# Performance work log

Measured on AMD Instinct MI355X. Metric: run time of the kernel, lower is better.

## Reference

```python
import jax, jax.numpy as jnp
import numpy as np

N_HEAD = 16


def setup_inputs() -> dict:
    key = jax.random.key(0)
    ks = jax.random.split(key, 4)
    B, S, E = 1, 4096, 1024
    x = jax.random.normal(ks[0], (B, S, E), dtype=jnp.float32)
    # causal mask: True where attention is DISALLOWED (upper triangle)
    masked_matrix = ~jnp.tril(jnp.ones((S, S), dtype=bool))[None, None]
    Wqkv = jax.random.normal(ks[1], (E, 3 * E), dtype=jnp.float32) * (1.0 / np.sqrt(E))
    bqkv = jnp.zeros((3 * E,), dtype=jnp.float32)
    Wp = jax.random.normal(ks[2], (E, E), dtype=jnp.float32) * (1.0 / np.sqrt(E))
    bp = jnp.zeros((E,), dtype=jnp.float32)
    return {"x": x, "masked_matrix": masked_matrix, "Wqkv": Wqkv, "bqkv": bqkv,
            "Wp": Wp, "bp": bp}


def reference(x, masked_matrix, Wqkv, bqkv, Wp, bp):
    B, S, E = x.shape
    H = N_HEAD
    D = E // H
    qkv = x @ Wqkv + bqkv                        # [B,S,3E]
    q, k, v = jnp.split(qkv, 3, axis=-1)
    q = q.reshape(B, S, H, D).transpose(0, 2, 1, 3)  # [B,H,S,D]
    k = k.reshape(B, S, H, D).transpose(0, 2, 1, 3)
    v = v.reshape(B, S, H, D).transpose(0, 2, 1, 3)
    # NOTE: source applies NO 1/sqrt(D) scaling — kept faithful.
    att = jnp.einsum('bhqd,bhkd->bhqk', q, k)    # [B,H,S,S]
    att = jnp.where(masked_matrix, jnp.float32(-jnp.inf), att)
    att = jax.nn.softmax(att, axis=-1)
    res = jnp.einsum('bhqk,bhkd->bhqd', att, v)  # [B,H,S,D]
    res = res.transpose(0, 2, 1, 3).reshape(B, S, E)
    return res @ Wp + bp
```

## Files before the change

### kernel.cpp

```cpp
#include <hip/hip_runtime.h>
#include <hip/hip_bf16.h>
#include <math.h>

#define S_LEN 4096
#define EMB   1024
#define NHEAD 16
#define HDIM  64

typedef __attribute__((ext_vector_type(8))) _Float16 half8;
typedef __attribute__((ext_vector_type(4))) _Float16 half4;
typedef __attribute__((ext_vector_type(4))) float float4_t;
typedef __attribute__((ext_vector_type(16))) float float16_t;
typedef __attribute__((ext_vector_type(4))) int int4_t;
typedef __attribute__((ext_vector_type(2))) int int2_t;

#define GLOBAL_AS(p) ((const __attribute__((address_space(1))) void*)(p))
#define LDS_AS(p)    ((__attribute__((address_space(3))) void*)(p))

#define LOG2E 1.4426950408889634f

__global__ __launch_bounds__(256) void prep(
    const float* __restrict__ x, const float* __restrict__ Wqkv,
    const float* __restrict__ Wp,
    _Float16* __restrict__ xh, _Float16* __restrict__ WTh,
    _Float16* __restrict__ WpT)
{
    const int bid = blockIdx.x;
    if (bid < 4096) {
        const int i = bid * 256 + threadIdx.x;
        const float4_t v = ((const float4_t*)x)[i];
        half4 hh;
#pragma unroll
        for (int j = 0; j < 4; ++j) hh[j] = (_Float16)v[j];
        ((half4*)xh)[i] = hh;
        return;
    }
    __shared__ float t[64][65];
    const float* in;
    _Float16* out;
    int R, C, bx, by;
    if (bid < 4096 + 768) {
        const int idx = bid - 4096;
        bx = idx % 48; by = idx / 48;
        in = Wqkv; out = WTh; R = 1024; C = 3072;
    } else {
        const int idx = bid - 4864;
        bx = idx & 15; by = idx >> 4;
        in = Wp; out = WpT; R = 1024; C = 1024;
    }
    const int r0 = by * 64, c0 = bx * 64;
    for (int i = threadIdx.x; i < 64 * 64; i += 256) {
        int r = i >> 6, c = i & 63;
        t[r][c] = in[(size_t)(r0 + r) * C + c0 + c];
    }
    __syncthreads();
    for (int i = threadIdx.x; i < 64 * 64; i += 256) {
        int c = i >> 6, r = i & 63;
        out[(size_t)(c0 + c) * R + r0 + r] = (_Float16)t[r][c];
    }
}

__global__ __launch_bounds__(256) void gemm_qkv(
    const _Float16* __restrict__ Ag, const _Float16* __restrict__ Bg,
    const float* __restrict__ bias,
    _Float16* __restrict__ qk, _Float16* __restrict__ vt, int K)
{
    constexpr int BK = 32;
    __shared__ _Float16 Ah[128 * BK];
    __shared__ _Float16 Bh[128 * BK];

    const int tid = threadIdx.x;
    const int wave = tid >> 6, lane = tid & 63;
    const int l16 = lane & 15, quad = lane >> 4;
    const int wr = wave >> 1, wc = wave & 1;
    const int row0 = blockIdx.y * 128, col0 = blockIdx.x * 128;
    const int lrow = lane >> 2, lc8 = (lane & 3) * 8;

    float4_t acc[4][4];
#pragma unroll
    for (int i = 0; i < 4; ++i)
#pragma unroll
        for (int j = 0; j < 4; ++j) acc[i][j] = (float4_t){0.f, 0.f, 0.f, 0.f};

    for (int k0 = 0; k0 < K; k0 += BK) {
        __syncthreads();
#pragma unroll
        for (int i = 0; i < 2; ++i) {
            const int ar = i * 64 + wave * 16;
            __builtin_amdgcn_global_load_lds(
                GLOBAL_AS(Ag + (size_t)(row0 + ar + lrow) * K + k0 + lc8),
                LDS_AS(&Ah[ar * BK]), 16, 0, 0);
            __builtin_amdgcn_global_load_lds(
                GLOBAL_AS(Bg + (size_t)(col0 + ar + lrow) * K + k0 + lc8),
                LDS_AS(&Bh[ar * BK]), 16, 0, 0);
        }
        __syncthreads();

        half8 af[4], bfr[4];
#pragma unroll
        for (int t = 0; t < 4; ++t) {
            af[t]  = *(const half8*)&Ah[(wr * 64 + t * 16 + l16) * BK + quad * 8];
            bfr[t] = *(const half8*)&Bh[(wc * 64 + t * 16 + l16) * BK + quad * 8];
        }
#pragma unroll
        for (int i = 0; i < 4; ++i)
#pragma unroll
            for (int j = 0; j < 4; ++j)
                acc[i][j] = __builtin_amdgcn_mfma_f32_16x16x32_f16(af[i], bfr[j], acc[i][j], 0, 0, 0);
    }

#pragma unroll
    for (int i = 0; i < 4; ++i) {
#pragma unroll
        for (int j = 0; j < 4; ++j) {
            const int colb = col0 + wc * 64 + j * 16 + l16;
            const float bv = bias[colb];
            const int rowb = row0 + wr * 64 + i * 16 + quad * 4;
            if (colb < 2048) {
                const float sc = (colb >= 1024) ? LOG2E : 1.0f;
#pragma unroll
                for (int r = 0; r < 4; ++r)
                    qk[(size_t)(rowb + r) * 2048 + colb] =
                        (_Float16)((acc[i][j][r] + bv) * sc);
            } else {
                half4 w;
#pragma unroll
                for (int r = 0; r < 4; ++r) w[r] = (_Float16)(acc[i][j][r] + bv);
                *(half4*)&vt[(size_t)(colb - 2048) * 4096 + rowb] = w;
            }
        }
    }
}

__global__ __launch_bounds__(256) void gemm_out(
    const _Float16* __restrict__ Ag, const _Float16* __restrict__ Bg,
    const float* __restrict__ bias, float* __restrict__ C, int N, int K)
{
    constexpr int BK = 32;
    __shared__ _Float16 Ah[128 * BK];
    __shared__ _Float16 Bh[64 * BK];

    const int tid = threadIdx.x;
    const int wave = tid >> 6, lane = tid & 63;
    const int l16 = lane & 15, quad = lane >> 4;
    const int row0 = blockIdx.y * 128, col0 = blockIdx.x * 64;
    const int lrow = lane >> 2, lc8 = (lane & 3) * 8;

    float4_t acc[2][4];
#pragma unroll
    for (int i = 0; i < 2; ++i)
#pragma unroll
        for (int j = 0; j < 4; ++j) acc[i][j] = (float4_t){0.f, 0.f, 0.f, 0.f};

    for (int k0 = 0; k0 < K; k0 += BK) {
        __syncthreads();
#pragma unroll
        for (int i = 0; i < 2; ++i) {
            const int ar = i * 64 + wave * 16;
            __builtin_amdgcn_global_load_lds(
                GLOBAL_AS(Ag + (size_t)(row0 + ar + lrow) * K + k0 + lc8),
                LDS_AS(&Ah[ar * BK]), 16, 0, 0);
        }
        {
            const int br = wave * 16;
            __builtin_amdgcn_global_load_lds(
                GLOBAL_AS(Bg + (size_t)(col0 + br + lrow) * K + k0 + lc8),
                LDS_AS(&Bh[br * BK]), 16, 0, 0);
        }
        __syncthreads();

        half8 af[2], bfr[4];
#pragma unroll
        for (int t = 0; t < 2; ++t)
            af[t] = *(const half8*)&Ah[(wave * 32 + t * 16 + l16) * BK + quad * 8];
#pragma unroll
        for (int t = 0; t < 4; ++t)
            bfr[t] = *(const half8*)&Bh[(t * 16 + l16) * BK + quad * 8];
#pragma unroll
        for (int i = 0; i < 2; ++i)
#pragma unroll
            for (int j = 0; j < 4; ++j)
                acc[i][j] = __builtin_amdgcn_mfma_f32_16x16x32_f16(af[i], bfr[j], acc[i][j], 0, 0, 0);
    }

#pragma unroll
    for (int i = 0; i < 2; ++i) {
#pragma unroll
        for (int j = 0; j < 4; ++j) {
            const int colb = col0 + j * 16 + l16;
            const float bv = bias[colb];
#pragma unroll
            for (int r = 0; r < 4; ++r) {
                const int row = row0 + wave * 32 + i * 16 + quad * 4 + r;
                C[(size_t)row * N + colb] = acc[i][j][r] + bv;
            }
        }
    }
}

__global__ __launch_bounds__(256, 4) void flash_attn_f16(
    const _Float16* __restrict__ qk, const _Float16* __restrict__ v_t,
    _Float16* __restrict__ opart, float* __restrict__ mlpart)
{
    __shared__ __align__(16) _Float16 KsT[2][64 * 64];
    __shared__ __align__(16) _Float16 VtT[2][64 * 64];

    const int bid  = blockIdx.x;
    const int g    = bid & 255;
    const int hv   = g & 15;
    const int h    = (hv & 7) * 2 + (hv >> 3);
    const int j    = g >> 4;
    const int v    = bid >> 8;
    const int tile = (v & 1) ? (31 - j) : j;
    const int split= v >> 1;

    const int wave = threadIdx.x >> 6;
    const int lane = threadIdx.x & 63;
    const int l31  = lane & 31;
    const int hi   = lane >> 5;

    const int dma_r = wave * 16 + (lane >> 3);
    const int dma_c = ((lane & 7) ^ (lane >> 3)) * 8;

    const _Float16* kplane = qk + 1024 + h * HDIM;
    const _Float16* vplane = v_t + (size_t)h * HDIM * 4096;

    const int q0 = tile * 128 + wave * 32;

    half8 qf[4];
#pragma unroll
    for (int jj = 0; jj < 4; ++jj)
        qf[jj] = *(const half8*)(qk + (size_t)(q0 + l31) * 2048 + h * HDIM
                                 + jj * 16 + hi * 8);

    float16_t o0 = (float16_t)0.f, o1 = (float16_t)0.f;
    float m_r = -INFINITY, l_r = 0.f;

    const int kb0 = 64 * split;
#pragma unroll
    for (int p = 0; p < 2; ++p) {
        const int r = dma_r + p * 8;
        __builtin_amdgcn_global_load_lds(
            GLOBAL_AS(kplane + (size_t)(kb0 + r) * 2048 + dma_c),
            LDS_AS(&KsT[0][(wave * 128 + p * 64) * 8]), 16, 0, 0);
        __builtin_amdgcn_global_load_lds(
            GLOBAL_AS(vplane + (size_t)r * 4096 + kb0 + dma_c),
            LDS_AS(&VtT[0][(wave * 128 + p * 64) * 8]), 16, 0, 0);
    }

    int ib = 0;
    int kb = kb0;
    for (int it = 0; it <= tile; ++it, kb += 128, ib ^= 1) {
        __syncthreads();

        if (it < tile) {
            const int kn = kb + 128;
#pragma unroll
            for (int p = 0; p < 2; ++p) {
                const int r = dma_r + p * 8;
                __builtin_amdgcn_global_load_lds(
                    GLOBAL_AS(kplane + (size_t)(kn + r) * 2048 + dma_c),
                    LDS_AS(&KsT[ib ^ 1][(wave * 128 + p * 64) * 8]), 16, 0, 0);
                __builtin_amdgcn_global_load_lds(
                    GLOBAL_AS(vplane + (size_t)r * 4096 + kn + dma_c),
                    LDS_AS(&VtT[ib ^ 1][(wave * 128 + p * 64) * 8]), 16, 0, 0);
            }
        }

        if (kb <= q0 + 31) {
            float16_t s0 = (float16_t)0.f, s1 = (float16_t)0.f;
            __builtin_amdgcn_s_setprio(1);
#pragma unroll
            for (int jj = 0; jj < 4; ++jj) {
                const int r7 = l31 & 7;
                const half8 kf0 = *(const half8*)&KsT[ib][
                    ((l31) * 8 + ((2 * jj + hi) ^ r7)) * 8];
                const half8 kf1 = *(const half8*)&KsT[ib][
                    ((32 + l31) * 8 + ((2 * jj + hi) ^ r7)) * 8];
                s0 = __builtin_amdgcn_mfma_f32_32x32x16_f16(kf0, qf[jj], s0, 0, 0, 0);
                s1 = __builtin_amdgcn_mfma_f32_32x32x16_f16(kf1, qf[jj], s1, 0, 0, 0);
            }
            __builtin_amdgcn_s_setprio(0);

            if (kb + 63 > q0) {
                const int qg = q0 + l31;
#pragma unroll
                for (int gg = 0; gg < 4; ++gg)
#pragma unroll
                    for (int r = 0; r < 4; ++r) {
                        const int keyb = kb + r + 8 * gg + 4 * hi;
                        if (keyb > qg)      s0[4 * gg + r] = -INFINITY;
                        if (keyb + 32 > qg) s1[4 * gg + r] = -INFINITY;
                    }
            }

            float mx = s0[0];
#pragma unroll
            for (int i = 1; i < 16; ++i) mx = fmaxf(mx, s0[i]);
#pragma unroll
            for (int i = 0; i < 16; ++i) mx = fmaxf(mx, s1[i]);
            mx = fmaxf(mx, __shfl_xor(mx, 32));
            const bool  grow  = mx > m_r + 8.0f;
            const float mnew  = grow ? mx : m_r;
            const float alpha = __builtin_amdgcn_exp2f(m_r - mnew);

            int w0[8], w1[8];
            float lsum = 0.f;
#pragma unroll
            for (int i = 0; i < 8; ++i) {
                const float pa = __builtin_amdgcn_exp2f(s0[2 * i]     - mnew);
                const float pb = __builtin_amdgcn_exp2f(s0[2 * i + 1] - mnew);
                lsum += pa + pb;
                w0[i] = __builtin_bit_cast(int, __builtin_amdgcn_cvt_pkrtz(pa, pb));
            }
#pragma unroll
            for (int i = 0; i < 8; ++i) {
                const float pa = __builtin_amdgcn_exp2f(s1[2 * i]     - mnew);
                const float pb = __builtin_amdgcn_exp2f(s1[2 * i + 1] - mnew);
                lsum += pa + pb;
                w1[i] = __builtin_bit_cast(int, __builtin_amdgcn_cvt_pkrtz(pa, pb));
            }
            l_r = l_r * alpha + lsum;
            m_r = mnew;
            if (__any(grow)) {
#pragma unroll
                for (int i = 0; i < 16; ++i) { o0[i] *= alpha; o1[i] *= alpha; }
            }

            half8 pf[4];
            {
                const int2_t a02 = __builtin_amdgcn_permlane32_swap(w0[0], w0[2], 0, 0);
                const int2_t a13 = __builtin_amdgcn_permlane32_swap(w0[1], w0[3], 0, 0);
                const int2_t a46 = __builtin_amdgcn_permlane32_swap(w0[4], w0[6], 0, 0);
                const int2_t a57 = __builtin_amdgcn_permlane32_swap(w0[5], w0[7], 0, 0);
                int4_t f0 = {a02[0], a13[0], a02[1], a13[1]};
                int4_t f1 = {a46[0], a57[0], a46[1], a57[1]};
                pf[0] = __builtin_bit_cast(half8, f0);
                pf[1] = __builtin_bit_cast(half8, f1);
                const int2_t b02 = __builtin_amdgcn_permlane32_swap(w1[0], w1[2], 0, 0);
                const int2_t b13 = __builtin_amdgcn_permlane32_swap(w1[1], w1[3], 0, 0);
                const int2_t b46 = __builtin_amdgcn_permlane32_swap(w1[4], w1[6], 0, 0);
                const int2_t b57 = __builtin_amdgcn_permlane32_swap(w1[5], w1[7], 0, 0);
                int4_t f2 = {b02[0], b13[0], b02[1], b13[1]};
                int4_t f3 = {b46[0], b57[0], b46[1], b57[1]};
                pf[2] = __builtin_bit_cast(half8, f2);
                pf[3] = __builtin_bit_cast(half8, f3);
            }

            __builtin_amdgcn_s_setprio(1);
#pragma unroll
            for (int kc = 0; kc < 4; ++kc) {
                const int r7 = l31 & 7;
                const half8 vf0 = *(const half8*)&VtT[ib][
                    ((l31) * 8 + ((2 * kc + hi) ^ r7)) * 8];
                const half8 vf1 = *(const half8*)&VtT[ib][
                    ((32 + l31) * 8 + ((2 * kc + hi) ^ r7)) * 8];
                o0 = __builtin_amdgcn_mfma_f32_32x32x16_f16(vf0, pf[kc], o0, 0, 0, 0);
                o1 = __builtin_amdgcn_mfma_f32_32x32x16_f16(vf1, pf[kc], o1, 0, 0, 0);
            }
            __builtin_amdgcn_s_setprio(0);
        }
    }

    const float lr = l_r + __shfl_xor(l_r, 32);
    const size_t prow = (size_t)(split * 4096 + q0 + l31);
#pragma unroll
    for (int gg = 0; gg < 4; ++gg) {
        half4 wa, wb;
#pragma unroll
        for (int r = 0; r < 4; ++r) {
            wa[r] = (_Float16)o0[4 * gg + r];
            wb[r] = (_Float16)o1[4 * gg + r];
        }
        const size_t base = prow * 1024 + h * HDIM + 8 * gg + 4 * hi;
        *(half4*)&opart[base]      = wa;
        *(half4*)&opart[base + 32] = wb;
    }
    if (hi == 0) {
        float2 ml; ml.x = m_r; ml.y = lr;
        ((float2*)mlpart)[prow * 16 + h] = ml;
    }
}

__global__ __launch_bounds__(256) void combine(
    const _Float16* __restrict__ opart, const float* __restrict__ mlpart,
    _Float16* __restrict__ resh)
{
    const int idx = blockIdx.x * 256 + threadIdx.x;
    const int row = idx >> 7;
    const int c8  = (idx & 127) * 8;
    const int h   = c8 >> 6;
    const float2 ml0 = ((const float2*)mlpart)[(size_t)row * 16 + h];
    const float2 ml1 = ((const float2*)mlpart)[(size_t)(4096 + row) * 16 + h];
    const float m  = fmaxf(ml0.x, ml1.x);
    const float a0 = __builtin_amdgcn_exp2f(ml0.x - m);
    const float a1 = __builtin_amdgcn_exp2f(ml1.x - m);
    const float inv = 1.0f / (ml0.y * a0 + ml1.y * a1);
    const half8 o0 = *(const half8*)&opart[(size_t)row * 1024 + c8];
    const half8 o1 = *(const half8*)&opart[(size_t)(4096 + row) * 1024 + c8];
    half8 w;
#pragma unroll
    for (int jj = 0; jj < 8; ++jj)
        w[jj] = (_Float16)(((float)o0[jj] * a0 + (float)o1[jj] * a1) * inv);
    *(half8*)&resh[(size_t)row * 1024 + c8] = w;
}

extern "C" void kernel_launch(void* const* d_in, const int* in_sizes, int n_in,
                              void* d_out, int out_size, void* d_ws, size_t ws_size,
                              hipStream_t stream)
{
    const float* x    = (const float*)d_in[0];
    const float* Wqkv = (const float*)d_in[2];
    const float* bqkv = (const float*)d_in[3];
    const float* Wp   = (const float*)d_in[4];
    const float* bp   = (const float*)d_in[5];
    float* out = (float*)d_out;

    _Float16* xh  = (_Float16*)d_ws;
    _Float16* WTh = xh + (size_t)4096 * 1024;
    _Float16* qkh = WTh + (size_t)3072 * 1024;
    _Float16* vtg = qkh + (size_t)4096 * 2048;
    _Float16* WpT = vtg + (size_t)1024 * 4096;
    _Float16* opart = WpT + (size_t)1024 * 1024;
    float* mlpart = (float*)(opart + (size_t)2 * 4096 * 1024);
    _Float16* resh = xh;

    dim3 blk(256);

    prep<<<dim3(5120), blk, 0, stream>>>(x, Wqkv, Wp, xh, WTh, WpT);

    gemm_qkv<<<dim3(3072 / 128, 4096 / 128), blk, 0, stream>>>(
        xh, WTh, bqkv, qkh, vtg, 1024);

    flash_attn_f16<<<dim3(1024), dim3(256), 0, stream>>>(qkh, vtg, opart, mlpart);

    combine<<<dim3(2048), blk, 0, stream>>>(opart, mlpart, resh);

    gemm_out<<<dim3(1024 / 64, 4096 / 128), blk, 0, stream>>>(
        resh, WpT, bp, out, 1024, 1024);
}
```

Baseline: 245.6 us.

## Split flash attention KV range four ways and combine four partials

Raises the KV-split factor from 2 to 4: each block handles every fourth 64-key chunk of its query tile, the grid doubles to 2048 blocks ordered longest tile first, and the combine kernel merges four partial outputs. Launch bounds go to 5 blocks per SM. The aim is more parallelism and better load balance across CUs for the causal workload. In exchange it writes and reads twice as much partial output and m/l data, adds combine work, and may spill registers under the tighter occupancy bound. Blocks with no keys still write -inf/zero partials, which the combine handles through exp2 weighting.

Result: slower. 272.9 us (+11.1%).

```diff
diff --git a/kernel.cpp b/kernel.cpp
--- a/kernel.cpp
+++ b/kernel.cpp
@@ -198,7 +198,7 @@
     }
 }
 
-__global__ __launch_bounds__(256, 4) void flash_attn_f16(
+__global__ __launch_bounds__(256, 5) void flash_attn_f16(
     const _Float16* __restrict__ qk, const _Float16* __restrict__ v_t,
     _Float16* __restrict__ opart, float* __restrict__ mlpart)
 {
@@ -206,13 +206,13 @@
     __shared__ __align__(16) _Float16 VtT[2][64 * 64];
 
     const int bid  = blockIdx.x;
-    const int g    = bid & 255;
-    const int hv   = g & 15;
+    const int hv   = bid & 15;
     const int h    = (hv & 7) * 2 + (hv >> 3);
-    const int j    = g >> 4;
-    const int v    = bid >> 8;
-    const int tile = (v & 1) ? (31 - j) : j;
-    const int split= v >> 1;
+    const int idx  = bid >> 4;
+    const int tile = 31 - (idx >> 2);
+    const int split= idx & 3;
+    const int dlen = 2 * tile + 1 - split;
+    const int L    = (dlen < 0) ? 0 : (dlen >> 2) + 1;
 
     const int wave = threadIdx.x >> 6;
     const int lane = threadIdx.x & 63;
@@ -236,129 +236,131 @@
     float16_t o0 = (float16_t)0.f, o1 = (float16_t)0.f;
     float m_r = -INFINITY, l_r = 0.f;
 
-    const int kb0 = 64 * split;
-#pragma unroll
-    for (int p = 0; p < 2; ++p) {
-        const int r = dma_r + p * 8;
-        __builtin_amdgcn_global_load_lds(
-            GLOBAL_AS(kplane + (size_t)(kb0 + r) * 2048 + dma_c),
-            LDS_AS(&KsT[0][(wave * 128 + p * 64) * 8]), 16, 0, 0);
-        __builtin_amdgcn_global_load_lds(
-            GLOBAL_AS(vplane + (size_t)r * 4096 + kb0 + dma_c),
-            LDS_AS(&VtT[0][(wave * 128 + p * 64) * 8]), 16, 0, 0);
-    }
-
-    int ib = 0;
-    int kb = kb0;
-    for (int it = 0; it <= tile; ++it, kb += 128, ib ^= 1) {
-        __syncthreads();
-
-        if (it < tile) {
-            const int kn = kb + 128;
-#pragma unroll
-            for (int p = 0; p < 2; ++p) {
-                const int r = dma_r + p * 8;
-                __builtin_amdgcn_global_load_lds(
-                    GLOBAL_AS(kplane + (size_t)(kn + r) * 2048 + dma_c),
-                    LDS_AS(&KsT[ib ^ 1][(wave * 128 + p * 64) * 8]), 16, 0, 0);
-                __builtin_amdgcn_global_load_lds(
-                    GLOBAL_AS(vplane + (size_t)r * 4096 + kn + dma_c),
-                    LDS_AS(&VtT[ib ^ 1][(wave * 128 + p * 64) * 8]), 16, 0, 0);
+    if (L > 0) {
+        const int kb0 = 64 * split;
+#pragma unroll
+        for (int p = 0; p < 2; ++p) {
+            const int r = dma_r + p * 8;
+            __builtin_amdgcn_global_load_lds(
+                GLOBAL_AS(kplane + (size_t)(kb0 + r) * 2048 + dma_c),
+                LDS_AS(&KsT[0][(wave * 128 + p * 64) * 8]), 16, 0, 0);
+            __builtin_amdgcn_global_load_lds(
+                GLOBAL_AS(vplane + (size_t)r * 4096 + kb0 + dma_c),
+                LDS_AS(&VtT[0][(wave * 128 + p * 64) * 8]), 16, 0, 0);
+        }
+
+        int ib = 0;
+        int kb = kb0;
+        for (int it = 0; it < L; ++it, kb += 256, ib ^= 1) {
+            __syncthreads();
+
+            if (it < L - 1) {
+                const int kn = kb + 256;
+#pragma unroll
+                for (int p = 0; p < 2; ++p) {
+                    const int r = dma_r + p * 8;
+                    __builtin_amdgcn_global_load_lds(
+                        GLOBAL_AS(kplane + (size_t)(kn + r) * 2048 + dma_c),
+                        LDS_AS(&KsT[ib ^ 1][(wave * 128 + p * 64) * 8]), 16, 0, 0);
+                    __builtin_amdgcn_global_load_lds(
+                        GLOBAL_AS(vplane + (size_t)r * 4096 + kn + dma_c),
+                        LDS_AS(&VtT[ib ^ 1][(wave * 128 + p * 64) * 8]), 16, 0, 0);
+                }
             }
-        }
-
-        if (kb <= q0 + 31) {
-            float16_t s0 = (float16_t)0.f, s1 = (float16_t)0.f;
-            __builtin_amdgcn_s_setprio(1);
-#pragma unroll
-            for (int jj = 0; jj < 4; ++jj) {
-                const int r7 = l31 & 7;
-                const half8 kf0 = *(const half8*)&KsT[ib][
-                    ((l31) * 8 + ((2 * jj + hi) ^ r7)) * 8];
-                const half8 kf1 = *(const half8*)&KsT[ib][
-                    ((32 + l31) * 8 + ((2 * jj + hi) ^ r7)) * 8];
-                s0 = __builtin_amdgcn_mfma_f32_32x32x16_f16(kf0, qf[jj], s0, 0, 0, 0);
-                s1 = __builtin_amdgcn_mfma_f32_32x32x16_f16(kf1, qf[jj], s1, 0, 0, 0);
+
+            if (kb <= q0 + 31) {
+                float16_t s0 = (float16_t)0.f, s1 = (float16_t)0.f;
+                __builtin_amdgcn_s_setprio(1);
+#pragma unroll
+                for (int jj = 0; jj < 4; ++jj) {
+                    const int r7 = l31 & 7;
+                    const half8 kf0 = *(const half8*)&KsT[ib][
+                        ((l31) * 8 + ((2 * jj + hi) ^ r7)) * 8];
+                    const half8 kf1 = *(const half8*)&KsT[ib][
+                        ((32 + l31) * 8 + ((2 * jj + hi) ^ r7)) * 8];
+                    s0 = __builtin_amdgcn_mfma_f32_32x32x16_f16(kf0, qf[jj], s0, 0, 0, 0);
+                    s1 = __builtin_amdgcn_mfma_f32_32x32x16_f16(kf1, qf[jj], s1, 0, 0, 0);
+                }
+                __builtin_amdgcn_s_setprio(0);
+
+                if (kb + 63 > q0) {
+                    const int qg = q0 + l31;
+#pragma unroll
+                    for (int gg = 0; gg < 4; ++gg)
+#pragma unroll
+                        for (int r = 0; r < 4; ++r) {
+                            const int keyb = kb + r + 8 * gg + 4 * hi;
+                            if (keyb > qg)      s0[4 * gg + r] = -INFINITY;
+                            if (keyb + 32 > qg) s1[4 * gg + r] = -INFINITY;
+                        }
+                }
+
+                float mx = s0[0];
+#pragma unroll
+                for (int i = 1; i < 16; ++i) mx = fmaxf(mx, s0[i]);
+#pragma unroll
+                for (int i = 0; i < 16; ++i) mx = fmaxf(mx, s1[i]);
+                mx = fmaxf(mx, __shfl_xor(mx, 32));
+                const bool  grow  = mx > m_r + 8.0f;
+                const float mnew  = grow ? mx : m_r;
+                const float alpha = __builtin_amdgcn_exp2f(m_r - mnew);
+
+                int w0[8], w1[8];
+                float lsum = 0.f;
+#pragma unroll
+                for (int i = 0; i < 8; ++i) {
+                    const float pa = __builtin_amdgcn_exp2f(s0[2 * i]     - mnew);
+                    const float pb = __builtin_amdgcn_exp2f(s0[2 * i + 1] - mnew);
+                    lsum += pa + pb;
+                    w0[i] = __builtin_bit_cast(int, __builtin_amdgcn_cvt_pkrtz(pa, pb));
+                }
+#pragma unroll
+                for (int i = 0; i < 8; ++i) {
+                    const float pa = __builtin_amdgcn_exp2f(s1[2 * i]     - mnew);
+                    const float pb = __builtin_amdgcn_exp2f(s1[2 * i + 1] - mnew);
+                    lsum += pa + pb;
+                    w1[i] = __builtin_bit_cast(int, __builtin_amdgcn_cvt_pkrtz(pa, pb));
+                }
+                l_r = l_r * alpha + lsum;
+                m_r = mnew;
+                if (__any(grow)) {
+#pragma unroll
+                    for (int i = 0; i < 16; ++i) { o0[i] *= alpha; o1[i] *= alpha; }
+                }
+
+                half8 pf[4];
+                {
+                    const int2_t a02 = __builtin_amdgcn_permlane32_swap(w0[0], w0[2], 0, 0);
+                    const int2_t a13 = __builtin_amdgcn_permlane32_swap(w0[1], w0[3], 0, 0);
+                    const int2_t a46 = __builtin_amdgcn_permlane32_swap(w0[4], w0[6], 0, 0);
+                    const int2_t a57 = __builtin_amdgcn_permlane32_swap(w0[5], w0[7], 0, 0);
+                    int4_t f0 = {a02[0], a13[0], a02[1], a13[1]};
+                    int4_t f1 = {a46[0], a57[0], a46[1], a57[1]};
+                    pf[0] = __builtin_bit_cast(half8, f0);
+                    pf[1] = __builtin_bit_cast(half8, f1);
+                    const int2_t b02 = __builtin_amdgcn_permlane32_swap(w1[0], w1[2], 0, 0);
+                    const int2_t b13 = __builtin_amdgcn_permlane32_swap(w1[1], w1[3], 0, 0);
+                    const int2_t b46 = __builtin_amdgcn_permlane32_swap(w1[4], w1[6], 0, 0);
+                    const int2_t b57 = __builtin_amdgcn_permlane32_swap(w1[5], w1[7], 0, 0);
+                    int4_t f2 = {b02[0], b13[0], b02[1], b13[1]};
+                    int4_t f3 = {b46[0], b57[0], b46[1], b57[1]};
+                    pf[2] = __builtin_bit_cast(half8, f2);
+                    pf[3] = __builtin_bit_cast(half8, f3);
+                }
+
+                __builtin_amdgcn_s_setprio(1);
+#pragma unroll
+                for (int kc = 0; kc < 4; ++kc) {
+                    const int r7 = l31 & 7;
+                    const half8 vf0 = *(const half8*)&VtT[ib][
+                        ((l31) * 8 + ((2 * kc + hi) ^ r7)) * 8];
+                    const half8 vf1 = *(const half8*)&VtT[ib][
+                        ((32 + l31) * 8 + ((2 * kc + hi) ^ r7)) * 8];
+                    o0 = __builtin_amdgcn_mfma_f32_32x32x16_f16(vf0, pf[kc], o0, 0, 0, 0);
+                    o1 = __builtin_amdgcn_mfma_f32_32x32x16_f16(vf1, pf[kc], o1, 0, 0, 0);
+                }
+                __builtin_amdgcn_s_setprio(0);
             }
-            __builtin_amdgcn_s_setprio(0);
-
-            if (kb + 63 > q0) {
-                const int qg = q0 + l31;
-#pragma unroll
-                for (int gg = 0; gg < 4; ++gg)
-#pragma unroll
-                    for (int r = 0; r < 4; ++r) {
-                        const int keyb = kb + r + 8 * gg + 4 * hi;
-                        if (keyb > qg)      s0[4 * gg + r] = -INFINITY;
-                        if (keyb + 32 > qg) s1[4 * gg + r] = -INFINITY;
-                    }
-            }
-
-            float mx = s0[0];
-#pragma unroll
-            for (int i = 1; i < 16; ++i) mx = fmaxf(mx, s0[i]);
-#pragma unroll
-            for (int i = 0; i < 16; ++i) mx = fmaxf(mx, s1[i]);
-            mx = fmaxf(mx, __shfl_xor(mx, 32));
-            const bool  grow  = mx > m_r + 8.0f;
-            const float mnew  = grow ? mx : m_r;
-            const float alpha = __builtin_amdgcn_exp2f(m_r - mnew);
-
-            int w0[8], w1[8];
-            float lsum = 0.f;
-#pragma unroll
-            for (int i = 0; i < 8; ++i) {
-                const float pa = __builtin_amdgcn_exp2f(s0[2 * i]     - mnew);
-                const float pb = __builtin_amdgcn_exp2f(s0[2 * i + 1] - mnew);
-                lsum += pa + pb;
-                w0[i] = __builtin_bit_cast(int, __builtin_amdgcn_cvt_pkrtz(pa, pb));
-            }
-#pragma unroll
-            for (int i = 0; i < 8; ++i) {
-                const float pa = __builtin_amdgcn_exp2f(s1[2 * i]     - mnew);
-                const float pb = __builtin_amdgcn_exp2f(s1[2 * i + 1] - mnew);
-                lsum += pa + pb;
-                w1[i] = __builtin_bit_cast(int, __builtin_amdgcn_cvt_pkrtz(pa, pb));
-            }
-            l_r = l_r * alpha + lsum;
-            m_r = mnew;
-            if (__any(grow)) {
-#pragma unroll
-                for (int i = 0; i < 16; ++i) { o0[i] *= alpha; o1[i] *= alpha; }
-            }
-
-            half8 pf[4];
-            {
-                const int2_t a02 = __builtin_amdgcn_permlane32_swap(w0[0], w0[2], 0, 0);
-                const int2_t a13 = __builtin_amdgcn_permlane32_swap(w0[1], w0[3], 0, 0);
-                const int2_t a46 = __builtin_amdgcn_permlane32_swap(w0[4], w0[6], 0, 0);
-                const int2_t a57 = __builtin_amdgcn_permlane32_swap(w0[5], w0[7], 0, 0);
-                int4_t f0 = {a02[0], a13[0], a02[1], a13[1]};
-                int4_t f1 = {a46[0], a57[0], a46[1], a57[1]};
-                pf[0] = __builtin_bit_cast(half8, f0);
-                pf[1] = __builtin_bit_cast(half8, f1);
-                const int2_t b02 = __builtin_amdgcn_permlane32_swap(w1[0], w1[2], 0, 0);
-                const int2_t b13 = __builtin_amdgcn_permlane32_swap(w1[1], w1[3], 0, 0);
-                const int2_t b46 = __builtin_amdgcn_permlane32_swap(w1[4], w1[6], 0, 0);
-                const int2_t b57 = __builtin_amdgcn_permlane32_swap(w1[5], w1[7], 0, 0);
-                int4_t f2 = {b02[0], b13[0], b02[1], b13[1]};
-                int4_t f3 = {b46[0], b57[0], b46[1], b57[1]};
-                pf[2] = __builtin_bit_cast(half8, f2);
-                pf[3] = __builtin_bit_cast(half8, f3);
-            }
-
-            __builtin_amdgcn_s_setprio(1);
-#pragma unroll
-            for (int kc = 0; kc < 4; ++kc) {
-                const int r7 = l31 & 7;
-                const half8 vf0 = *(const half8*)&VtT[ib][
-                    ((l31) * 8 + ((2 * kc + hi) ^ r7)) * 8];
-                const half8 vf1 = *(const half8*)&VtT[ib][
-                    ((32 + l31) * 8 + ((2 * kc + hi) ^ r7)) * 8];
-                o0 = __builtin_amdgcn_mfma_f32_32x32x16_f16(vf0, pf[kc], o0, 0, 0, 0);
-                o1 = __builtin_amdgcn_mfma_f32_32x32x16_f16(vf1, pf[kc], o1, 0, 0, 0);
-            }
-            __builtin_amdgcn_s_setprio(0);
         }
     }
 
@@ -390,18 +392,30 @@
     const int row = idx >> 7;
     const int c8  = (idx & 127) * 8;
     const int h   = c8 >> 6;
-    const float2 ml0 = ((const float2*)mlpart)[(size_t)row * 16 + h];
-    const float2 ml1 = ((const float2*)mlpart)[(size_t)(4096 + row) * 16 + h];
-    const float m  = fmaxf(ml0.x, ml1.x);
-    const float a0 = __builtin_amdgcn_exp2f(ml0.x - m);
-    const float a1 = __builtin_amdgcn_exp2f(ml1.x - m);
-    const float inv = 1.0f / (ml0.y * a0 + ml1.y * a1);
-    const half8 o0 = *(const half8*)&opart[(size_t)row * 1024 + c8];
-    const half8 o1 = *(const half8*)&opart[(size_t)(4096 + row) * 1024 + c8];
+    float2 ml[4];
+#pragma unroll
+    for (int s = 0; s < 4; ++s)
+        ml[s] = ((const float2*)mlpart)[(size_t)(s * 4096 + row) * 16 + h];
+    const float m = fmaxf(fmaxf(ml[0].x, ml[1].x), fmaxf(ml[2].x, ml[3].x));
+    float a[4], lsum = 0.f;
+#pragma unroll
+    for (int s = 0; s < 4; ++s) {
+        a[s] = __builtin_amdgcn_exp2f(ml[s].x - m);
+        lsum += ml[s].y * a[s];
+    }
+    const float inv = 1.0f / lsum;
+    float acc[8];
+#pragma unroll
+    for (int jj = 0; jj < 8; ++jj) acc[jj] = 0.f;
+#pragma unroll
+    for (int s = 0; s < 4; ++s) {
+        const half8 os = *(const half8*)&opart[(size_t)(s * 4096 + row) * 1024 + c8];
+#pragma unroll
+        for (int jj = 0; jj < 8; ++jj) acc[jj] += (float)os[jj] * a[s];
+    }
     half8 w;
 #pragma unroll
-    for (int jj = 0; jj < 8; ++jj)
-        w[jj] = (_Float16)(((float)o0[jj] * a0 + (float)o1[jj] * a1) * inv);
+    for (int jj = 0; jj < 8; ++jj) w[jj] = (_Float16)(acc[jj] * inv);
     *(half8*)&resh[(size_t)row * 1024 + c8] = w;
 }
 
@@ -422,7 +436,7 @@
     _Float16* vtg = qkh + (size_t)4096 * 2048;
     _Float16* WpT = vtg + (size_t)1024 * 4096;
     _Float16* opart = WpT + (size_t)1024 * 1024;
-    float* mlpart = (float*)(opart + (size_t)2 * 4096 * 1024);
+    float* mlpart = (float*)(opart + (size_t)4 * 4096 * 1024);
     _Float16* resh = xh;
 
     dim3 blk(256);
@@ -432,7 +446,7 @@
     gemm_qkv<<<dim3(3072 / 128, 4096 / 128), blk, 0, stream>>>(
         xh, WTh, bqkv, qkh, vtg, 1024);
 
-    flash_attn_f16<<<dim3(1024), dim3(256), 0, stream>>>(qkh, vtg, opart, mlpart);
+    flash_attn_f16<<<dim3(2048), dim3(256), 0, stream>>>(qkh, vtg, opart, mlpart);
 
     combine<<<dim3(2048), blk, 0, stream>>>(opart, mlpart, resh);
 
```

## Process two KV tiles per barrier in flash attention and swizzle GEMM block order

Applied to the files above, without the earlier changes.

The flash attention loop now stages two 64-key K/V tiles per double-buffer slot. Each __syncthreads therefore covers two tiles, which halves the number of barriers. LDS use doubles to 64KB and the occupancy hint drops from 4 to 2 blocks per CU. Both GEMMs remap block indices with a grouped swizzle to improve L2 reuse, and the softmax max and sum reductions become tree-shaped to shorten dependency chains.

New measurement: 252.7 us. 1.03x slower.

```diff
diff --git a/kernel.cpp b/kernel.cpp
--- a/kernel.cpp
+++ b/kernel.cpp
@@ -73,7 +73,9 @@
     const int wave = tid >> 6, lane = tid & 63;
     const int l16 = lane & 15, quad = lane >> 4;
     const int wr = wave >> 1, wc = wave & 1;
-    const int row0 = blockIdx.y * 128, col0 = blockIdx.x * 128;
+    const int lid = blockIdx.y * 24 + blockIdx.x;
+    const int swz = (lid & 7) * 96 + (lid >> 3);
+    const int row0 = (swz / 24) * 128, col0 = (swz % 24) * 128;
     const int lrow = lane >> 2, lc8 = (lane & 3) * 8;
 
     float4_t acc[4][4];
@@ -143,7 +145,9 @@
     const int tid = threadIdx.x;
     const int wave = tid >> 6, lane = tid & 63;
     const int l16 = lane & 15, quad = lane >> 4;
-    const int row0 = blockIdx.y * 128, col0 = blockIdx.x * 64;
+    const int lid = blockIdx.y * 16 + blockIdx.x;
+    const int swz = (lid & 7) * 64 + (lid >> 3);
+    const int row0 = (swz / 16) * 128, col0 = (swz % 16) * 64;
     const int lrow = lane >> 2, lc8 = (lane & 3) * 8;
 
     float4_t acc[2][4];
@@ -198,12 +202,12 @@
     }
 }
 
-__global__ __launch_bounds__(256, 4) void flash_attn_f16(
+__global__ __launch_bounds__(256, 2) void flash_attn_f16(
     const _Float16* __restrict__ qk, const _Float16* __restrict__ v_t,
     _Float16* __restrict__ opart, float* __restrict__ mlpart)
 {
-    __shared__ __align__(16) _Float16 KsT[2][64 * 64];
-    __shared__ __align__(16) _Float16 VtT[2][64 * 64];
+    __shared__ __align__(16) _Float16 KsT[2][2][64 * 64];
+    __shared__ __align__(16) _Float16 VtT[2][2][64 * 64];
 
     const int bid  = blockIdx.x;
     const int g    = bid & 255;
@@ -237,129 +241,139 @@
     float m_r = -INFINITY, l_r = 0.f;
 
     const int kb0 = 64 * split;
-#pragma unroll
-    for (int p = 0; p < 2; ++p) {
-        const int r = dma_r + p * 8;
-        __builtin_amdgcn_global_load_lds(
-            GLOBAL_AS(kplane + (size_t)(kb0 + r) * 2048 + dma_c),
-            LDS_AS(&KsT[0][(wave * 128 + p * 64) * 8]), 16, 0, 0);
-        __builtin_amdgcn_global_load_lds(
-            GLOBAL_AS(vplane + (size_t)r * 4096 + kb0 + dma_c),
-            LDS_AS(&VtT[0][(wave * 128 + p * 64) * 8]), 16, 0, 0);
-    }
+    const int L   = tile + 1;
+    const int S   = (L + 1) >> 1;
+
+    auto stage1 = [&](int ibuf, int sub, int kbv) {
+#pragma unroll
+        for (int p = 0; p < 2; ++p) {
+            const int r = dma_r + p * 8;
+            __builtin_amdgcn_global_load_lds(
+                GLOBAL_AS(kplane + (size_t)(kbv + r) * 2048 + dma_c),
+                LDS_AS(&KsT[ibuf][sub][(wave * 128 + p * 64) * 8]), 16, 0, 0);
+            __builtin_amdgcn_global_load_lds(
+                GLOBAL_AS(vplane + (size_t)r * 4096 + kbv + dma_c),
+                LDS_AS(&VtT[ibuf][sub][(wave * 128 + p * 64) * 8]), 16, 0, 0);
+        }
+    };
+
+    auto body = [&](int ibuf, int sub, int kb) {
+        if (kb > q0 + 31) return;
+        const _Float16* Ks = &KsT[ibuf][sub][0];
+        const _Float16* Vs = &VtT[ibuf][sub][0];
+
+        float16_t s0 = (float16_t)0.f, s1 = (float16_t)0.f;
+        __builtin_amdgcn_s_setprio(1);
+#pragma unroll
+        for (int jj = 0; jj < 4; ++jj) {
+            const int r7 = l31 & 7;
+            const half8 kf0 = *(const half8*)&Ks[((l31) * 8 + ((2 * jj + hi) ^ r7)) * 8];
+            const half8 kf1 = *(const half8*)&Ks[((32 + l31) * 8 + ((2 * jj + hi) ^ r7)) * 8];
+            s0 = __builtin_amdgcn_mfma_f32_32x32x16_f16(kf0, qf[jj], s0, 0, 0, 0);
+            s1 = __builtin_amdgcn_mfma_f32_32x32x16_f16(kf1, qf[jj], s1, 0, 0, 0);
+        }
+        __builtin_amdgcn_s_setprio(0);
+
+        if (kb + 63 > q0) {
+            const int qg = q0 + l31;
+#pragma unroll
+            for (int gg = 0; gg < 4; ++gg)
+#pragma unroll
+                for (int r = 0; r < 4; ++r) {
+                    const int keyb = kb + r + 8 * gg + 4 * hi;
+                    if (keyb > qg)      s0[4 * gg + r] = -INFINITY;
+                    if (keyb + 32 > qg) s1[4 * gg + r] = -INFINITY;
+                }
+        }
+
+        float a0 = fmaxf(s0[0], s0[1]),  a1 = fmaxf(s0[2], s0[3]);
+        float a2 = fmaxf(s0[4], s0[5]),  a3 = fmaxf(s0[6], s0[7]);
+        float a4 = fmaxf(s0[8], s0[9]),  a5 = fmaxf(s0[10], s0[11]);
+        float a6 = fmaxf(s0[12], s0[13]), a7 = fmaxf(s0[14], s0[15]);
+        float b0 = fmaxf(s1[0], s1[1]),  b1 = fmaxf(s1[2], s1[3]);
+        float b2 = fmaxf(s1[4], s1[5]),  b3 = fmaxf(s1[6], s1[7]);
+        float b4 = fmaxf(s1[8], s1[9]),  b5 = fmaxf(s1[10], s1[11]);
+        float b6 = fmaxf(s1[12], s1[13]), b7 = fmaxf(s1[14], s1[15]);
+        a0 = fmaxf(a0, a1); a2 = fmaxf(a2, a3); a4 = fmaxf(a4, a5); a6 = fmaxf(a6, a7);
+        b0 = fmaxf(b0, b1); b2 = fmaxf(b2, b3); b4 = fmaxf(b4, b5); b6 = fmaxf(b6, b7);
+        a0 = fmaxf(a0, a2); a4 = fmaxf(a4, a6); b0 = fmaxf(b0, b2); b4 = fmaxf(b4, b6);
+        float mx = fmaxf(fmaxf(a0, a4), fmaxf(b0, b4));
+        mx = fmaxf(mx, __shfl_xor(mx, 32));
+        const bool  grow  = mx > m_r + 8.0f;
+        const float mnew  = grow ? mx : m_r;
+        const float alpha = __builtin_amdgcn_exp2f(m_r - mnew);
+
+        int w0[8], w1[8];
+        float ls0 = 0.f, ls1 = 0.f, ls2 = 0.f, ls3 = 0.f;
+#pragma unroll
+        for (int i = 0; i < 8; ++i) {
+            const float pa = __builtin_amdgcn_exp2f(s0[2 * i]     - mnew);
+            const float pb = __builtin_amdgcn_exp2f(s0[2 * i + 1] - mnew);
+            if (i & 1) ls1 += pa + pb; else ls0 += pa + pb;
+            w0[i] = __builtin_bit_cast(int, __builtin_amdgcn_cvt_pkrtz(pa, pb));
+        }
+#pragma unroll
+        for (int i = 0; i < 8; ++i) {
+            const float pa = __builtin_amdgcn_exp2f(s1[2 * i]     - mnew);
+            const float pb = __builtin_amdgcn_exp2f(s1[2 * i + 1] - mnew);
+            if (i & 1) ls3 += pa + pb; else ls2 += pa + pb;
+            w1[i] = __builtin_bit_cast(int, __builtin_amdgcn_cvt_pkrtz(pa, pb));
+        }
+        const float lsum = (ls0 + ls1) + (ls2 + ls3);
+        l_r = l_r * alpha + lsum;
+        m_r = mnew;
+        if (__any(grow)) {
+#pragma unroll
+            for (int i = 0; i < 16; ++i) { o0[i] *= alpha; o1[i] *= alpha; }
+        }
+
+        half8 pf[4];
+        {
+            const int2_t c02 = __builtin_amdgcn_permlane32_swap(w0[0], w0[2], 0, 0);
+            const int2_t c13 = __builtin_amdgcn_permlane32_swap(w0[1], w0[3], 0, 0);
+            const int2_t c46 = __builtin_amdgcn_permlane32_swap(w0[4], w0[6], 0, 0);
+            const int2_t c57 = __builtin_amdgcn_permlane32_swap(w0[5], w0[7], 0, 0);
+            int4_t f0 = {c02[0], c13[0], c02[1], c13[1]};
+            int4_t f1 = {c46[0], c57[0], c46[1], c57[1]};
+            pf[0] = __builtin_bit_cast(half8, f0);
+            pf[1] = __builtin_bit_cast(half8, f1);
+            const int2_t d02 = __builtin_amdgcn_permlane32_swap(w1[0], w1[2], 0, 0);
+            const int2_t d13 = __builtin_amdgcn_permlane32_swap(w1[1], w1[3], 0, 0);
+            const int2_t d46 = __builtin_amdgcn_permlane32_swap(w1[4], w1[6], 0, 0);
+            const int2_t d57 = __builtin_amdgcn_permlane32_swap(w1[5], w1[7], 0, 0);
+            int4_t f2 = {d02[0], d13[0], d02[1], d13[1]};
+            int4_t f3 = {d46[0], d57[0], d46[1], d57[1]};
+            pf[2] = __builtin_bit_cast(half8, f2);
+            pf[3] = __builtin_bit_cast(half8, f3);
+        }
+
+        __builtin_amdgcn_s_setprio(1);
+#pragma unroll
+        for (int kc = 0; kc < 4; ++kc) {
+            const int r7 = l31 & 7;
+            const half8 vf0 = *(const half8*)&Vs[((l31) * 8 + ((2 * kc + hi) ^ r7)) * 8];
+            const half8 vf1 = *(const half8*)&Vs[((32 + l31) * 8 + ((2 * kc + hi) ^ r7)) * 8];
+            o0 = __builtin_amdgcn_mfma_f32_32x32x16_f16(vf0, pf[kc], o0, 0, 0, 0);
+            o1 = __builtin_amdgcn_mfma_f32_32x32x16_f16(vf1, pf[kc], o1, 0, 0, 0);
+        }
+        __builtin_amdgcn_s_setprio(0);
+    };
+
+    stage1(0, 0, kb0);
+    if (1 < L) stage1(0, 1, kb0 + 128);
 
     int ib = 0;
-    int kb = kb0;
-    for (int it = 0; it <= tile; ++it, kb += 128, ib ^= 1) {
+    for (int st = 0; st < S; ++st, ib ^= 1) {
         __syncthreads();
 
-        if (it < tile) {
-            const int kn = kb + 128;
-#pragma unroll
-            for (int p = 0; p < 2; ++p) {
-                const int r = dma_r + p * 8;
-                __builtin_amdgcn_global_load_lds(
-                    GLOBAL_AS(kplane + (size_t)(kn + r) * 2048 + dma_c),
-                    LDS_AS(&KsT[ib ^ 1][(wave * 128 + p * 64) * 8]), 16, 0, 0);
-                __builtin_amdgcn_global_load_lds(
-                    GLOBAL_AS(vplane + (size_t)r * 4096 + kn + dma_c),
-                    LDS_AS(&VtT[ib ^ 1][(wave * 128 + p * 64) * 8]), 16, 0, 0);
-            }
-        }
-
-        if (kb <= q0 + 31) {
-            float16_t s0 = (float16_t)0.f, s1 = (float16_t)0.f;
-            __builtin_amdgcn_s_setprio(1);
-#pragma unroll
-            for (int jj = 0; jj < 4; ++jj) {
-                const int r7 = l31 & 7;
-                const half8 kf0 = *(const half8*)&KsT[ib][
-                    ((l31) * 8 + ((2 * jj + hi) ^ r7)) * 8];
-                const half8 kf1 = *(const half8*)&KsT[ib][
-                    ((32 + l31) * 8 + ((2 * jj + hi) ^ r7)) * 8];
-                s0 = __builtin_amdgcn_mfma_f32_32x32x16_f16(kf0, qf[jj], s0, 0, 0, 0);
-                s1 = __builtin_amdgcn_mfma_f32_32x32x16_f16(kf1, qf[jj], s1, 0, 0, 0);
-            }
-            __builtin_amdgcn_s_setprio(0);
-
-            if (kb + 63 > q0) {
-                const int qg = q0 + l31;
-#pragma unroll
-                for (int gg = 0; gg < 4; ++gg)
-#pragma unroll
-                    for (int r = 0; r < 4; ++r) {
-                        const int keyb = kb + r + 8 * gg + 4 * hi;
-                        if (keyb > qg)      s0[4 * gg + r] = -INFINITY;
-                        if (keyb + 32 > qg) s1[4 * gg + r] = -INFINITY;
-                    }
-            }
-
-            float mx = s0[0];
-#pragma unroll
-            for (int i = 1; i < 16; ++i) mx = fmaxf(mx, s0[i]);
-#pragma unroll
-            for (int i = 0; i < 16; ++i) mx = fmaxf(mx, s1[i]);
-            mx = fmaxf(mx, __shfl_xor(mx, 32));
-            const bool  grow  = mx > m_r + 8.0f;
-            const float mnew  = grow ? mx : m_r;
-            const float alpha = __builtin_amdgcn_exp2f(m_r - mnew);
-
-            int w0[8], w1[8];
-            float lsum = 0.f;
-#pragma unroll
-            for (int i = 0; i < 8; ++i) {
-                const float pa = __builtin_amdgcn_exp2f(s0[2 * i]     - mnew);
-                const float pb = __builtin_amdgcn_exp2f(s0[2 * i + 1] - mnew);
-                lsum += pa + pb;
-                w0[i] = __builtin_bit_cast(int, __builtin_amdgcn_cvt_pkrtz(pa, pb));
-            }
-#pragma unroll
-            for (int i = 0; i < 8; ++i) {
-                const float pa = __builtin_amdgcn_exp2f(s1[2 * i]     - mnew);
-                const float pb = __builtin_amdgcn_exp2f(s1[2 * i + 1] - mnew);
-                lsum += pa + pb;
-                w1[i] = __builtin_bit_cast(int, __builtin_amdgcn_cvt_pkrtz(pa, pb));
-            }
-            l_r = l_r * alpha + lsum;
-            m_r = mnew;
-            if (__any(grow)) {
-#pragma unroll
-                for (int i = 0; i < 16; ++i) { o0[i] *= alpha; o1[i] *= alpha; }
-            }
-
-            half8 pf[4];
-            {
-                const int2_t a02 = __builtin_amdgcn_permlane32_swap(w0[0], w0[2], 0, 0);
-                const int2_t a13 = __builtin_amdgcn_permlane32_swap(w0[1], w0[3], 0, 0);
-                const int2_t a46 = __builtin_amdgcn_permlane32_swap(w0[4], w0[6], 0, 0);
-                const int2_t a57 = __builtin_amdgcn_permlane32_swap(w0[5], w0[7], 0, 0);
-                int4_t f0 = {a02[0], a13[0], a02[1], a13[1]};
-                int4_t f1 = {a46[0], a57[0], a46[1], a57[1]};
-                pf[0] = __builtin_bit_cast(half8, f0);
-                pf[1] = __builtin_bit_cast(half8, f1);
-                const int2_t b02 = __builtin_amdgcn_permlane32_swap(w1[0], w1[2], 0, 0);
-                const int2_t b13 = __builtin_amdgcn_permlane32_swap(w1[1], w1[3], 0, 0);
-                const int2_t b46 = __builtin_amdgcn_permlane32_swap(w1[4], w1[6], 0, 0);
-                const int2_t b57 = __builtin_amdgcn_permlane32_swap(w1[5], w1[7], 0, 0);
-                int4_t f2 = {b02[0], b13[0], b02[1], b13[1]};
-                int4_t f3 = {b46[0], b57[0], b46[1], b57[1]};
-                pf[2] = __builtin_bit_cast(half8, f2);
-                pf[3] = __builtin_bit_cast(half8, f3);
-            }
-
-            __builtin_amdgcn_s_setprio(1);
-#pragma unroll
-            for (int kc = 0; kc < 4; ++kc) {
-                const int r7 = l31 & 7;
-                const half8 vf0 = *(const half8*)&VtT[ib][
-                    ((l31) * 8 + ((2 * kc + hi) ^ r7)) * 8];
-                const half8 vf1 = *(const half8*)&VtT[ib][
-                    ((32 + l31) * 8 + ((2 * kc + hi) ^ r7)) * 8];
-                o0 = __builtin_amdgcn_mfma_f32_32x32x16_f16(vf0, pf[kc], o0, 0, 0, 0);
-                o1 = __builtin_amdgcn_mfma_f32_32x32x16_f16(vf1, pf[kc], o1, 0, 0, 0);
-            }
-            __builtin_amdgcn_s_setprio(0);
-        }
+        if (st + 1 < S) {
+            const int i2 = 2 * (st + 1);
+            stage1(ib ^ 1, 0, kb0 + 128 * i2);
+            if (i2 + 1 < L) stage1(ib ^ 1, 1, kb0 + 128 * (i2 + 1));
+        }
+
+        body(ib, 0, kb0 + 256 * st);
+        if (2 * st + 1 < L) body(ib, 1, kb0 + 256 * st + 128);
     }
 
     const float lr = l_r + __shfl_xor(l_r, 32);
```

## Double GEMM K-tile, XOR-swizzle LDS, remap blocks per XCD, stage epilogue stores

Applied to the files above, without the earlier changes.

Both projection GEMMs now load 64-wide K tiles per iteration, which halves the number of barrier-separated loop trips. The LDS tiles use an XOR swizzle on 16-byte chunks to avoid bank conflicts on the fragment reads. Block indices are remapped so that neighbouring tiles land on the same XCD, which should improve L2 reuse. The QKV epilogue is staged through shared memory so that both q/k and the transposed V are written with coalesced 16-byte stores. The cost is more LDS per block and hardcoded grid-shape assumptions in the block remapping.

Measured after the change: 234.8 us. 1.05x faster.

```diff
diff --git a/kernel.cpp b/kernel.cpp
--- a/kernel.cpp
+++ b/kernel.cpp
@@ -65,16 +65,22 @@
     const float* __restrict__ bias,
     _Float16* __restrict__ qk, _Float16* __restrict__ vt, int K)
 {
-    constexpr int BK = 32;
-    __shared__ _Float16 Ah[128 * BK];
-    __shared__ _Float16 Bh[128 * BK];
+    constexpr int BK = 64;
+    __shared__ __align__(16) _Float16 smem[128 * 136];
+    _Float16* Ah = smem;
+    _Float16* Bh = smem + 128 * 64;
+    auto Tq = (_Float16(*)[136])smem;
 
     const int tid = threadIdx.x;
     const int wave = tid >> 6, lane = tid & 63;
     const int l16 = lane & 15, quad = lane >> 4;
     const int wr = wave >> 1, wc = wave & 1;
-    const int row0 = blockIdx.y * 128, col0 = blockIdx.x * 128;
-    const int lrow = lane >> 2, lc8 = (lane & 3) * 8;
+    const int lid = blockIdx.y * 24 + blockIdx.x;
+    const int xcd = lid & 7, idx = lid >> 3;
+    const int row0 = ((xcd >> 1) * 8 + (idx & 7)) * 128;
+    const int col0 = ((xcd & 1) * 12 + (idx >> 3)) * 128;
+    const int srow = lane >> 3;
+    const int sc8  = ((lane & 7) ^ (srow & 7)) * 8;
 
     float4_t acc[4][4];
 #pragma unroll
@@ -85,49 +91,76 @@
     for (int k0 = 0; k0 < K; k0 += BK) {
         __syncthreads();
 #pragma unroll
-        for (int i = 0; i < 2; ++i) {
-            const int ar = i * 64 + wave * 16;
+        for (int i = 0; i < 4; ++i) {
+            const int ar = i * 32 + wave * 8;
             __builtin_amdgcn_global_load_lds(
-                GLOBAL_AS(Ag + (size_t)(row0 + ar + lrow) * K + k0 + lc8),
-                LDS_AS(&Ah[ar * BK]), 16, 0, 0);
+                GLOBAL_AS(Ag + (size_t)(row0 + ar + srow) * K + k0 + sc8),
+                LDS_AS(&Ah[ar * 64]), 16, 0, 0);
             __builtin_amdgcn_global_load_lds(
-                GLOBAL_AS(Bg + (size_t)(col0 + ar + lrow) * K + k0 + lc8),
-                LDS_AS(&Bh[ar * BK]), 16, 0, 0);
+                GLOBAL_AS(Bg + (size_t)(col0 + ar + srow) * K + k0 + sc8),
+                LDS_AS(&Bh[ar * 64]), 16, 0, 0);
         }
         __syncthreads();
 
-        half8 af[4], bfr[4];
+        half8 af[4][2], bfr[4][2];
 #pragma unroll
         for (int t = 0; t < 4; ++t) {
-            af[t]  = *(const half8*)&Ah[(wr * 64 + t * 16 + l16) * BK + quad * 8];
-            bfr[t] = *(const half8*)&Bh[(wc * 64 + t * 16 + l16) * BK + quad * 8];
-        }
-#pragma unroll
-        for (int i = 0; i < 4; ++i)
-#pragma unroll
-            for (int j = 0; j < 4; ++j)
-                acc[i][j] = __builtin_amdgcn_mfma_f32_16x16x32_f16(af[i], bfr[j], acc[i][j], 0, 0, 0);
-    }
-
+#pragma unroll
+            for (int ks = 0; ks < 2; ++ks) {
+                const int ra = wr * 64 + t * 16 + l16;
+                const int rb = wc * 64 + t * 16 + l16;
+                const int cc = ks * 4 + quad;
+                af[t][ks]  = *(const half8*)&Ah[ra * 64 + ((cc ^ (ra & 7))) * 8];
+                bfr[t][ks] = *(const half8*)&Bh[rb * 64 + ((cc ^ (rb & 7))) * 8];
+            }
+        }
+#pragma unroll
+        for (int ks = 0; ks < 2; ++ks)
+#pragma unroll
+            for (int i = 0; i < 4; ++i)
+#pragma unroll
+                for (int j = 0; j < 4; ++j)
+                    acc[i][j] = __builtin_amdgcn_mfma_f32_16x16x32_f16(
+                        af[i][ks], bfr[j][ks], acc[i][j], 0, 0, 0);
+    }
+
+    __syncthreads();
+    const bool  isV = (col0 >= 2048);
+    const float sc  = (col0 >= 1024 && col0 < 2048) ? LOG2E : 1.0f;
 #pragma unroll
     for (int i = 0; i < 4; ++i) {
 #pragma unroll
         for (int j = 0; j < 4; ++j) {
-            const int colb = col0 + wc * 64 + j * 16 + l16;
-            const float bv = bias[colb];
-            const int rowb = row0 + wr * 64 + i * 16 + quad * 4;
-            if (colb < 2048) {
-                const float sc = (colb >= 1024) ? LOG2E : 1.0f;
+            const int col = wc * 64 + j * 16 + l16;
+            const float bv = bias[col0 + col];
+            const int row = wr * 64 + i * 16 + quad * 4;
+            if (isV) {
 #pragma unroll
                 for (int r = 0; r < 4; ++r)
-                    qk[(size_t)(rowb + r) * 2048 + colb] =
-                        (_Float16)((acc[i][j][r] + bv) * sc);
+                    Tq[col][row + r] = (_Float16)(acc[i][j][r] + bv);
             } else {
-                half4 w;
-#pragma unroll
-                for (int r = 0; r < 4; ++r) w[r] = (_Float16)(acc[i][j][r] + bv);
-                *(half4*)&vt[(size_t)(colb - 2048) * 4096 + rowb] = w;
-            }
+#pragma unroll
+                for (int r = 0; r < 4; ++r)
+                    Tq[row + r][col] = (_Float16)((acc[i][j][r] + bv) * sc);
+            }
+        }
+    }
+    __syncthreads();
+    if (isV) {
+        _Float16* base = vt + (size_t)(col0 - 2048) * 4096 + row0;
+#pragma unroll
+        for (int pass = 0; pass < 8; ++pass) {
+            const int c  = pass * 16 + (tid >> 4);
+            const int ch = (tid & 15) * 8;
+            *(half8*)&base[(size_t)c * 4096 + ch] = *(const half8*)&Tq[c][ch];
+        }
+    } else {
+        _Float16* base = qk + (size_t)row0 * 2048 + col0;
+#pragma unroll
+        for (int pass = 0; pass < 8; ++pass) {
+            const int r  = pass * 16 + (tid >> 4);
+            const int ch = (tid & 15) * 8;
+            *(half8*)&base[(size_t)r * 2048 + ch] = *(const half8*)&Tq[r][ch];
         }
     }
 }
@@ -136,15 +169,18 @@
     const _Float16* __restrict__ Ag, const _Float16* __restrict__ Bg,
     const float* __restrict__ bias, float* __restrict__ C, int N, int K)
 {
-    constexpr int BK = 32;
-    __shared__ _Float16 Ah[128 * BK];
-    __shared__ _Float16 Bh[64 * BK];
+    constexpr int BK = 64;
+    __shared__ __align__(16) _Float16 Ah[128 * 64];
+    __shared__ __align__(16) _Float16 Bh[64 * 64];
 
     const int tid = threadIdx.x;
     const int wave = tid >> 6, lane = tid & 63;
     const int l16 = lane & 15, quad = lane >> 4;
-    const int row0 = blockIdx.y * 128, col0 = blockIdx.x * 64;
-    const int lrow = lane >> 2, lc8 = (lane & 3) * 8;
+    const int lid = blockIdx.y * 16 + blockIdx.x;
+    const int swz = (lid & 7) * 64 + (lid >> 3);
+    const int row0 = (swz / 16) * 128, col0 = (swz % 16) * 64;
+    const int srow = lane >> 3;
+    const int sc8  = ((lane & 7) ^ (srow & 7)) * 8;
 
     float4_t acc[2][4];
 #pragma unroll
@@ -155,32 +191,45 @@
     for (int k0 = 0; k0 < K; k0 += BK) {
         __syncthreads();
 #pragma unroll
+        for (int i = 0; i < 4; ++i) {
+            const int ar = i * 32 + wave * 8;
+            __builtin_amdgcn_global_load_lds(
+                GLOBAL_AS(Ag + (size_t)(row0 + ar + srow) * K + k0 + sc8),
+                LDS_AS(&Ah[ar * 64]), 16, 0, 0);
+        }
+#pragma unroll
         for (int i = 0; i < 2; ++i) {
-            const int ar = i * 64 + wave * 16;
+            const int br = i * 32 + wave * 8;
             __builtin_amdgcn_global_load_lds(
-                GLOBAL_AS(Ag + (size_t)(row0 + ar + lrow) * K + k0 + lc8),
-                LDS_AS(&Ah[ar * BK]), 16, 0, 0);
-        }
-        {
-            const int br = wave * 16;
-            __builtin_amdgcn_global_load_lds(
-                GLOBAL_AS(Bg + (size_t)(col0 + br + lrow) * K + k0 + lc8),
-                LDS_AS(&Bh[br * BK]), 16, 0, 0);
+                GLOBAL_AS(Bg + (size_t)(col0 + br + srow) * K + k0 + sc8),
+                LDS_AS(&Bh[br * 64]), 16, 0, 0);
         }
         __syncthreads();
 
-        half8 af[2], bfr[4];
-#pragma unroll
-        for (int t = 0; t < 2; ++t)
-            af[t] = *(const half8*)&Ah[(wave * 32 + t * 16 + l16) * BK + quad * 8];
-#pragma unroll
-        for (int t = 0; t < 4; ++t)
-            bfr[t] = *(const half8*)&Bh[(t * 16 + l16) * BK + quad * 8];
-#pragma unroll
-        for (int i = 0; i < 2; ++i)
-#pragma unroll
-            for (int j = 0; j < 4; ++j)
-                acc[i][j] = __builtin_amdgcn_mfma_f32_16x16x32_f16(af[i], bfr[j], acc[i][j], 0, 0, 0);
+        half8 af[2][2], bfr[4][2];
+#pragma unroll
+        for (int ks = 0; ks < 2; ++ks) {
+#pragma unroll
+            for (int t = 0; t < 2; ++t) {
+                const int ra = wave * 32 + t * 16 + l16;
+                const int cc = ks * 4 + quad;
+                af[t][ks] = *(const half8*)&Ah[ra * 64 + ((cc ^ (ra & 7))) * 8];
+            }
+#pragma unroll
+            for (int t = 0; t < 4; ++t) {
+                const int rb = t * 16 + l16;
+                const int cc = ks * 4 + quad;
+                bfr[t][ks] = *(const half8*)&Bh[rb * 64 + ((cc ^ (rb & 7))) * 8];
+            }
+        }
+#pragma unroll
+        for (int ks = 0; ks < 2; ++ks)
+#pragma unroll
+            for (int i = 0; i < 2; ++i)
+#pragma unroll
+                for (int j = 0; j < 4; ++j)
+                    acc[i][j] = __builtin_amdgcn_mfma_f32_16x16x32_f16(
+                        af[i][ks], bfr[j][ks], acc[i][j], 0, 0, 0);
     }
 
 #pragma unroll
```
